# Kernel tuning notes

Hardware: AMD Instinct MI355X
Metric: run time of the kernel (lower is better)

The kernel has to match this reference:

```python
import jax, jax.numpy as jnp
import numpy as np

B, C, Q, E = 32, 1024, 64, 256  # batch, max_context_len, max_question_len, embedding_size
FE = 4 * E                      # final_encoding_size (self_attention=False)


def setup_inputs() -> dict:
    key = jax.random.key(0)
    ks = jax.random.split(key, 7)
    return {
        "context": jax.random.normal(ks[0], (B, C, E), dtype=jnp.float32),
        "question": jax.random.normal(ks[1], (B, Q, E), dtype=jnp.float32),
        "context_mask": jnp.ones((B, C), dtype=jnp.float32),
        "w_question": jax.random.normal(ks[2], (E,), dtype=jnp.float32),
        "w_context": jax.random.normal(ks[3], (E,), dtype=jnp.float32),
        "w_multiple": jax.random.normal(ks[4], (E,), dtype=jnp.float32),
        "final_W": jax.random.normal(ks[5], (FE, FE), dtype=jnp.float32) * (1.0 / np.sqrt(FE)),
        "final_b": jnp.zeros((FE,), dtype=jnp.float32),
    }


def reference(context, question, context_mask, w_question, w_context, w_multiple, final_W, final_b):
    # Trilinear similarity: s[b,c,q] = <w_q, q_q> + <w_c, c_c> + <w_m, c_c * q_q>
    q_weighted = question @ w_question                 # (B, Q)
    ctx_weighted = context @ w_context                 # (B, C)
    # (question.unsqueeze(1) * context.unsqueeze(2)) @ w_multiple, computed
    # without materializing the (B, C, Q, E) intermediate:
    mult = jnp.einsum('bce,bqe->bcq', context * w_multiple, question)  # (B, C, Q)
    similarity = ctx_weighted[:, :, None] + q_weighted[:, None, :] + mult  # (B, C, Q)

    # Context-to-query attention (softmax over question dim)
    c2q_att = jnp.einsum('bcq,bqe->bce', jax.nn.softmax(similarity, axis=2), question)

    # Query-to-context attention (softmax over context dim of row-max scores)
    q2c_weights = jax.nn.softmax(jnp.max(similarity, axis=2), axis=1)   # (B, C)
    q2c_att = jnp.einsum('bc,bce->be', q2c_weights, context)            # (B, E)

    attended = jnp.concatenate(
        [context, c2q_att, context * c2q_att, context * q2c_att[:, None, :]],
        axis=2)                                                          # (B, C, 4E)

    # MaskedLinear: affine map, output rows zeroed where context_mask == 0
    out = (attended @ final_W.T + final_b) * context_mask[:, :, None]    # (B, C, 4E)
    return out
```

## Files before the change

### kernel.cpp

```cpp
#include <hip/hip_runtime.h>

#define BB 32
#define CC 1024
#define QQ 64
#define EE 256
#define FE 1024
#define MM (BB*CC)

typedef __bf16 bf16_t;
typedef bf16_t bf16x8 __attribute__((ext_vector_type(8)));
typedef float f32x4 __attribute__((ext_vector_type(4)));
typedef unsigned short u16x8 __attribute__((ext_vector_type(8)));

__device__ __forceinline__ unsigned short f2bf(float f) {
  unsigned u = __float_as_uint(f);
  u += 0x7fffu + ((u >> 16) & 1u);
  return (unsigned short)(u >> 16);
}
__device__ __forceinline__ float bf2f(unsigned short u) {
  return __uint_as_float(((unsigned)u) << 16);
}

__device__ __forceinline__ void gload_lds16(const void* g, void* l) {
  __builtin_amdgcn_global_load_lds(
      (const __attribute__((address_space(1))) unsigned int*)g,
      (__attribute__((address_space(3))) unsigned int*)l, 16, 0, 0);
}

__global__ void k_prep(const float* __restrict__ question, const float* __restrict__ w_question,
                       float* __restrict__ qw,
                       const float* __restrict__ W, unsigned short* __restrict__ Wb) {
  int bx = blockIdx.x;
  if (bx < 512) {
    int gid = bx * 256 + threadIdx.x;
    int row = gid >> 6;
    int lane = gid & 63;
    const float4 q = *(const float4*)(question + (size_t)row * EE + lane * 4);
    const float4 wq = *(const float4*)(w_question + lane * 4);
    float d = q.x*wq.x + q.y*wq.y + q.z*wq.z + q.w*wq.w;
    d += __shfl_xor(d, 1);  d += __shfl_xor(d, 2);  d += __shfl_xor(d, 4);
    d += __shfl_xor(d, 8);  d += __shfl_xor(d, 16); d += __shfl_xor(d, 32);
    if (lane == 0) qw[row] = d;
  } else {
    int i = ((bx - 512) * 256 + threadIdx.x) * 4;
    float4 v = *(const float4*)(W + i);
    ushort4 o; o.x = f2bf(v.x); o.y = f2bf(v.y); o.z = f2bf(v.z); o.w = f2bf(v.w);
    *(ushort4*)(Wb + i) = o;
  }
}

#define DOT4(acc, A, Bv) acc += A.x*Bv.x + A.y*Bv.y + A.z*Bv.z + A.w*Bv.w

__launch_bounds__(256)
__global__ void k_simpv(const float* __restrict__ ctx, const float* __restrict__ question,
                        const float* __restrict__ qw_g, const float* __restrict__ w_context,
                        const float* __restrict__ w_multiple,
                        float* __restrict__ rowmax, unsigned short* __restrict__ att) {
  __shared__ float qbuf[QQ * 132];
  __shared__ float ck[64][36];
  __shared__ unsigned short Pl[QQ][68];
  __shared__ float cwl[64];
  __shared__ float qwl[QQ];
  const int tid = threadIdx.x;
  const int b = blockIdx.y;
  const int c0 = blockIdx.x * 64;
  const int tx = tid & 15, ty = tid >> 4;

  const float* qb = question + (size_t)b * (QQ * EE);
  if (tid < QQ) qwl[tid] = qw_g[b * QQ + tid];

  const int cr = tid >> 3, er = (tid & 7) * 4;
  const float* crow0 = ctx + ((size_t)(b * CC + c0 + cr)) * EE;
  const float* crow1 = crow0 + 32 * EE;
  unsigned short* arow0 = att + ((size_t)(b * CC + c0 + cr)) * FE;
  unsigned short* arow1 = arow0 + (size_t)32 * FE;
  float s[4][4] = {{0.f}};
  float cp0 = 0.f, cp1 = 0.f;

  for (int h = 0; h < 2; ++h) {
    if (h) __syncthreads();
    for (int idx = tid * 4; idx < QQ * 128; idx += 1024) {
      int row = idx >> 7, col = idx & 127;
      *(float4*)&qbuf[row * 132 + col] = *(const float4*)(qb + (size_t)row * EE + h * 128 + col);
    }
    for (int eo2 = 0; eo2 < 128; eo2 += 32) {
      const int eo = h * 128 + eo2;
      float4 cv0 = *(const float4*)(crow0 + eo + er);
      float4 cv1 = *(const float4*)(crow1 + eo + er);
      float4 wc = *(const float4*)(w_context + eo + er);
      float4 wm = *(const float4*)(w_multiple + eo + er);
      cp0 += cv0.x*wc.x + cv0.y*wc.y + cv0.z*wc.z + cv0.w*wc.w;
      cp1 += cv1.x*wc.x + cv1.y*wc.y + cv1.z*wc.z + cv1.w*wc.w;
      ushort4 u0, u1;
      u0.x = f2bf(cv0.x); u0.y = f2bf(cv0.y); u0.z = f2bf(cv0.z); u0.w = f2bf(cv0.w);
      u1.x = f2bf(cv1.x); u1.y = f2bf(cv1.y); u1.z = f2bf(cv1.z); u1.w = f2bf(cv1.w);
      *(ushort4*)(arow0 + eo + er) = u0;
      *(ushort4*)(arow1 + eo + er) = u1;
      __syncthreads();
      float4 m0, m1;
      m0.x = cv0.x*wm.x; m0.y = cv0.y*wm.y; m0.z = cv0.z*wm.z; m0.w = cv0.w*wm.w;
      m1.x = cv1.x*wm.x; m1.y = cv1.y*wm.y; m1.z = cv1.z*wm.z; m1.w = cv1.w*wm.w;
      *(float4*)&ck[cr][er] = m0;
      *(float4*)&ck[cr + 32][er] = m1;
      __syncthreads();
#pragma unroll
      for (int ee = 0; ee < 32; ee += 4) {
        float4 a0 = *(const float4*)&ck[ty +  0][ee];
        float4 a1 = *(const float4*)&ck[ty + 16][ee];
        float4 a2 = *(const float4*)&ck[ty + 32][ee];
        float4 a3 = *(const float4*)&ck[ty + 48][ee];
        float4 b0 = *(const float4*)&qbuf[(tx +  0) * 132 + eo2 + ee];
        float4 b1 = *(const float4*)&qbuf[(tx + 16) * 132 + eo2 + ee];
        float4 b2 = *(const float4*)&qbuf[(tx + 32) * 132 + eo2 + ee];
        float4 b3 = *(const float4*)&qbuf[(tx + 48) * 132 + eo2 + ee];
        DOT4(s[0][0], a0, b0); DOT4(s[0][1], a0, b1); DOT4(s[0][2], a0, b2); DOT4(s[0][3], a0, b3);
        DOT4(s[1][0], a1, b0); DOT4(s[1][1], a1, b1); DOT4(s[1][2], a1, b2); DOT4(s[1][3], a1, b3);
        DOT4(s[2][0], a2, b0); DOT4(s[2][1], a2, b1); DOT4(s[2][2], a2, b2); DOT4(s[2][3], a2, b3);
        DOT4(s[3][0], a3, b0); DOT4(s[3][1], a3, b1); DOT4(s[3][2], a3, b2); DOT4(s[3][3], a3, b3);
      }
    }
  }
  cp0 += __shfl_xor(cp0, 1); cp0 += __shfl_xor(cp0, 2); cp0 += __shfl_xor(cp0, 4);
  cp1 += __shfl_xor(cp1, 1); cp1 += __shfl_xor(cp1, 2); cp1 += __shfl_xor(cp1, 4);
  if ((tid & 7) == 0) { cwl[cr] = cp0; cwl[cr + 32] = cp1; }
  __syncthreads();

#pragma unroll
  for (int i = 0; i < 4; ++i) {
    int c = ty + 16 * i;
    float cw = cwl[c];
    float f[4], mx = -1e30f;
#pragma unroll
    for (int j = 0; j < 4; ++j) {
      f[j] = s[i][j] + cw + qwl[tx + 16 * j];
      mx = fmaxf(mx, f[j]);
    }
    mx = fmaxf(mx, __shfl_xor(mx, 1));
    mx = fmaxf(mx, __shfl_xor(mx, 2));
    mx = fmaxf(mx, __shfl_xor(mx, 4));
    mx = fmaxf(mx, __shfl_xor(mx, 8));
    float sum = 0.f;
#pragma unroll
    for (int j = 0; j < 4; ++j) { f[j] = expf(f[j] - mx); sum += f[j]; }
    sum += __shfl_xor(sum, 1);
    sum += __shfl_xor(sum, 2);
    sum += __shfl_xor(sum, 4);
    sum += __shfl_xor(sum, 8);
    float inv = 1.f / sum;
    if (tx == 0) rowmax[(size_t)b * CC + c0 + c] = mx;
#pragma unroll
    for (int j = 0; j < 4; ++j) Pl[tx + 16 * j][c] = f2bf(f[j] * inv);
  }
  __syncthreads();

  for (int ep = 0; ep < EE; ep += 64) {
    if (ep) __syncthreads();
    {
      int q = tid >> 2, e16 = (tid & 3) * 16;
      const float* src = qb + (size_t)q * EE + ep + e16;
      *(float4*)&qbuf[q * 68 + e16 +  0] = *(const float4*)(src);
      *(float4*)&qbuf[q * 68 + e16 +  4] = *(const float4*)(src + 4);
      *(float4*)&qbuf[q * 68 + e16 +  8] = *(const float4*)(src + 8);
      *(float4*)&qbuf[q * 68 + e16 + 12] = *(const float4*)(src + 12);
    }
    __syncthreads();
    float s2[4][4] = {{0.f}};
#pragma unroll 8
    for (int q = 0; q < QQ; ++q) {
      float a0 = bf2f(Pl[q][ty +  0]);
      float a1 = bf2f(Pl[q][ty + 16]);
      float a2 = bf2f(Pl[q][ty + 32]);
      float a3 = bf2f(Pl[q][ty + 48]);
      float4 bv = *(const float4*)&qbuf[q * 68 + tx * 4];
      s2[0][0] += a0 * bv.x; s2[0][1] += a0 * bv.y; s2[0][2] += a0 * bv.z; s2[0][3] += a0 * bv.w;
      s2[1][0] += a1 * bv.x; s2[1][1] += a1 * bv.y; s2[1][2] += a1 * bv.z; s2[1][3] += a1 * bv.w;
      s2[2][0] += a2 * bv.x; s2[2][1] += a2 * bv.y; s2[2][2] += a2 * bv.z; s2[2][3] += a2 * bv.w;
      s2[3][0] += a3 * bv.x; s2[3][1] += a3 * bv.y; s2[3][2] += a3 * bv.z; s2[3][3] += a3 * bv.w;
    }
#pragma unroll
    for (int i = 0; i < 4; ++i) {
      int c = ty + 16 * i;
      size_t row = (size_t)(b * CC + c0 + c);
      unsigned short* arow = att + row * (size_t)FE;
      ushort4 cu = *(const ushort4*)(arow + ep + tx * 4);
      float cx = bf2f(cu.x), cy = bf2f(cu.y), cz = bf2f(cu.z), cw = bf2f(cu.w);
      ushort4 o1, o2;
      o1.x = f2bf(s2[i][0]);       o1.y = f2bf(s2[i][1]);       o1.z = f2bf(s2[i][2]);       o1.w = f2bf(s2[i][3]);
      o2.x = f2bf(cx * s2[i][0]);  o2.y = f2bf(cy * s2[i][1]);  o2.z = f2bf(cz * s2[i][2]);  o2.w = f2bf(cw * s2[i][3]);
      *(ushort4*)(arow + 1 * EE + ep + tx * 4) = o1;
      *(ushort4*)(arow + 2 * EE + ep + tx * 4) = o2;
    }
  }
}

__global__ void k_q2c_softmax(const float* __restrict__ rowmax, float* __restrict__ q2cw) {
  int b = blockIdx.x, tid = threadIdx.x;
  __shared__ float rbuf[4], sbuf[4];
  float4 v = *(const float4*)(rowmax + (size_t)b * CC + tid * 4);
  float m = fmaxf(fmaxf(v.x, v.y), fmaxf(v.z, v.w));
  for (int off = 1; off < 64; off <<= 1) m = fmaxf(m, __shfl_xor(m, off));
  int wv = tid >> 6;
  if ((tid & 63) == 0) rbuf[wv] = m;
  __syncthreads();
  m = fmaxf(fmaxf(rbuf[0], rbuf[1]), fmaxf(rbuf[2], rbuf[3]));
  float e0 = expf(v.x - m), e1 = expf(v.y - m), e2 = expf(v.z - m), e3 = expf(v.w - m);
  float sum = e0 + e1 + e2 + e3;
  for (int off = 1; off < 64; off <<= 1) sum += __shfl_xor(sum, off);
  if ((tid & 63) == 0) sbuf[wv] = sum;
  __syncthreads();
  sum = sbuf[0] + sbuf[1] + sbuf[2] + sbuf[3];
  float inv = 1.f / sum;
  float4 o; o.x = e0 * inv; o.y = e1 * inv; o.z = e2 * inv; o.w = e3 * inv;
  *(float4*)(q2cw + (size_t)b * CC + tid * 4) = o;
}

__global__ void k_q2c_part(const unsigned short* __restrict__ att, const float* __restrict__ w,
                           float* __restrict__ part) {
  int b = blockIdx.y, ch = blockIdx.x;
  int e = threadIdx.x;
  const unsigned short* base = att + ((size_t)(b * CC + ch * 128)) * FE + e;
  const float* wp = w + b * CC + ch * 128;
  float acc = 0.f;
#pragma unroll 4
  for (int c = 0; c < 128; ++c) acc += wp[c] * bf2f(base[(size_t)c * FE]);
  part[(b * 8 + ch) * EE + e] = acc;
}

__global__ void k_q2c_sum(const float* __restrict__ part, float* __restrict__ q2catt) {
  int b = blockIdx.x, e = threadIdx.x;
  float a = 0.f;
#pragma unroll
  for (int ch = 0; ch < 8; ++ch) a += part[(b * 8 + ch) * EE + e];
  q2catt[b * EE + e] = a;
}

__global__ void k_att3(const unsigned short* __restrict__ att_ro, const float* __restrict__ q2catt,
                       unsigned short* __restrict__ att_wr) {
  int unit = blockIdx.x * 256 + threadIdx.x;
  int row = unit >> 5;
  int e8 = (unit & 31) * 8;
  int b = row >> 10;
  u16x8 c = *(const u16x8*)(att_ro + (size_t)row * FE + e8);
  float4 g0 = *(const float4*)(q2catt + b * EE + e8);
  float4 g1 = *(const float4*)(q2catt + b * EE + e8 + 4);
  u16x8 o;
  o[0] = f2bf(bf2f(c[0]) * g0.x); o[1] = f2bf(bf2f(c[1]) * g0.y);
  o[2] = f2bf(bf2f(c[2]) * g0.z); o[3] = f2bf(bf2f(c[3]) * g0.w);
  o[4] = f2bf(bf2f(c[4]) * g1.x); o[5] = f2bf(bf2f(c[5]) * g1.y);
  o[6] = f2bf(bf2f(c[6]) * g1.z); o[7] = f2bf(bf2f(c[7]) * g1.w);
  *(u16x8*)(att_wr + (size_t)row * FE + 3 * EE + e8) = o;
}

__launch_bounds__(256, 3)
__global__ void k_gemm(const unsigned short* __restrict__ A, const unsigned short* __restrict__ Bw,
                       const float* __restrict__ bias, const float* __restrict__ mask,
                       float* __restrict__ out) {
  __shared__ bf16_t As[128][32];
  __shared__ bf16_t Bs[128][32];
  const int tid = threadIdx.x;
  const int lane = tid & 63;
  const int wave = tid >> 6;
  const int wr = wave >> 1, wc = wave & 1;

  const int bid = blockIdx.x;
  const int wg = (bid & 7) * 256 + (bid >> 3);
  const int bcol = (wg & 7) * 128;
  const int brow = (wg >> 3) * 128;

  const int r = lane & 15, kg = lane >> 4;
  const int rk = (kg ^ (r & 3)) * 8;

  const int srow = tid >> 2;
  const int sgr = tid & 3;
  const int ssw = (sgr ^ (srow & 3)) * 8;
  const unsigned short* gA0 = A  + (size_t)(brow + srow) * FE + ssw;
  const unsigned short* gA1 = gA0 + (size_t)64 * FE;
  const unsigned short* gB0 = Bw + (size_t)(bcol + srow) * FE + ssw;
  const unsigned short* gB1 = gB0 + (size_t)64 * FE;
  bf16_t* dA0 = &As[srow][sgr * 8];
  bf16_t* dA1 = dA0 + 64 * 32;
  bf16_t* dB0 = &Bs[srow][sgr * 8];
  bf16_t* dB1 = dB0 + 64 * 32;

  f32x4 acc[4][4] = {};

  for (int k0 = 0; k0 < FE; k0 += 32) {
    gload_lds16(gA0 + k0, dA0);
    gload_lds16(gA1 + k0, dA1);
    gload_lds16(gB0 + k0, dB0);
    gload_lds16(gB1 + k0, dB1);
    __syncthreads();
    bf16x8 fa[4], fb[4];
#pragma unroll
    for (int m = 0; m < 4; ++m) fa[m] = *(const bf16x8*)&As[wr * 64 + m * 16 + r][rk];
#pragma unroll
    for (int n = 0; n < 4; ++n) fb[n] = *(const bf16x8*)&Bs[wc * 64 + n * 16 + r][rk];
#pragma unroll
    for (int m = 0; m < 4; ++m)
#pragma unroll
      for (int n = 0; n < 4; ++n)
        acc[m][n] = __builtin_amdgcn_mfma_f32_16x16x32_bf16(fa[m], fb[n], acc[m][n], 0, 0, 0);
    __syncthreads();
  }

#pragma unroll
  for (int m = 0; m < 4; ++m) {
#pragma unroll
    for (int n = 0; n < 4; ++n) {
#pragma unroll
      for (int reg = 0; reg < 4; ++reg) {
        int row = brow + wr * 64 + m * 16 + kg * 4 + reg;
        int col = bcol + wc * 64 + n * 16 + r;
        out[(size_t)row * FE + col] = (acc[m][n][reg] + bias[col]) * mask[row];
      }
    }
  }
}

extern "C" void kernel_launch(void* const* d_in, const int* in_sizes, int n_in,
                              void* d_out, int out_size, void* d_ws, size_t ws_size,
                              hipStream_t stream) {
  const float* ctx  = (const float*)d_in[0];
  const float* ques = (const float*)d_in[1];
  const float* mask = (const float*)d_in[2];
  const float* w_q  = (const float*)d_in[3];
  const float* w_c  = (const float*)d_in[4];
  const float* w_m  = (const float*)d_in[5];
  const float* fW   = (const float*)d_in[6];
  const float* fb   = (const float*)d_in[7];
  float* out = (float*)d_out;

  char* ws = (char*)d_ws;
  float* qw     = (float*)(ws);
  float* rowmax = (float*)(ws + 8192);
  float* q2cw   = (float*)(ws + 139264);
  float* part   = (float*)(ws + 270336);
  float* q2catt = (float*)(ws + 532480);
  unsigned short* attended = (unsigned short*)(ws + 1048576);
  unsigned short* Wb       = (unsigned short*)(ws + 68157440);

  k_prep<<<1536, 256, 0, stream>>>(ques, w_q, qw, fW, Wb);
  k_simpv<<<dim3(16, 32), 256, 0, stream>>>(ctx, ques, qw, w_c, w_m, rowmax, attended);
  k_q2c_softmax<<<32, 256, 0, stream>>>(rowmax, q2cw);
  k_q2c_part<<<dim3(8, 32), 256, 0, stream>>>(attended, q2cw, part);
  k_q2c_sum<<<32, 256, 0, stream>>>(part, q2catt);
  k_att3<<<4096, 256, 0, stream>>>(attended, q2catt, attended);
  k_gemm<<<2048, 256, 0, stream>>>(attended, Wb, fb, mask, out);
}
```

Before: 172.2 us.

## Fuse q2c reduction and context*q2c scaling into GEMM A-tile load

Removes the k_q2c_sum and k_att3 kernels. Each GEMM block now sums the q2c partials for its batch into shared memory. For the last quarter of K it loads the context columns through registers, scales them by the q2c vector, and writes the result to LDS instead of using direct global-to-LDS loads. This saves two launches and one full read/write pass over a quarter of the attended buffer. In exchange, every GEMM block does redundant partial sums, and the register-path loads in the K loop are slower.

```diff
diff --git a/kernel.cpp b/kernel.cpp
--- a/kernel.cpp
+++ b/kernel.cpp
@@ -226,37 +226,13 @@
   part[(b * 8 + ch) * EE + e] = acc;
 }
 
-__global__ void k_q2c_sum(const float* __restrict__ part, float* __restrict__ q2catt) {
-  int b = blockIdx.x, e = threadIdx.x;
-  float a = 0.f;
-#pragma unroll
-  for (int ch = 0; ch < 8; ++ch) a += part[(b * 8 + ch) * EE + e];
-  q2catt[b * EE + e] = a;
-}
-
-__global__ void k_att3(const unsigned short* __restrict__ att_ro, const float* __restrict__ q2catt,
-                       unsigned short* __restrict__ att_wr) {
-  int unit = blockIdx.x * 256 + threadIdx.x;
-  int row = unit >> 5;
-  int e8 = (unit & 31) * 8;
-  int b = row >> 10;
-  u16x8 c = *(const u16x8*)(att_ro + (size_t)row * FE + e8);
-  float4 g0 = *(const float4*)(q2catt + b * EE + e8);
-  float4 g1 = *(const float4*)(q2catt + b * EE + e8 + 4);
-  u16x8 o;
-  o[0] = f2bf(bf2f(c[0]) * g0.x); o[1] = f2bf(bf2f(c[1]) * g0.y);
-  o[2] = f2bf(bf2f(c[2]) * g0.z); o[3] = f2bf(bf2f(c[3]) * g0.w);
-  o[4] = f2bf(bf2f(c[4]) * g1.x); o[5] = f2bf(bf2f(c[5]) * g1.y);
-  o[6] = f2bf(bf2f(c[6]) * g1.z); o[7] = f2bf(bf2f(c[7]) * g1.w);
-  *(u16x8*)(att_wr + (size_t)row * FE + 3 * EE + e8) = o;
-}
-
 __launch_bounds__(256, 3)
 __global__ void k_gemm(const unsigned short* __restrict__ A, const unsigned short* __restrict__ Bw,
-                       const float* __restrict__ bias, const float* __restrict__ mask,
-                       float* __restrict__ out) {
+                       const float* __restrict__ part, const float* __restrict__ bias,
+                       const float* __restrict__ mask, float* __restrict__ out) {
   __shared__ bf16_t As[128][32];
   __shared__ bf16_t Bs[128][32];
+  __shared__ float q2cl[EE];
   const int tid = threadIdx.x;
   const int lane = tid & 63;
   const int wave = tid >> 6;
@@ -266,6 +242,7 @@
   const int wg = (bid & 7) * 256 + (bid >> 3);
   const int bcol = (wg & 7) * 128;
   const int brow = (wg >> 3) * 128;
+  const int bb = brow >> 10;
 
   const int r = lane & 15, kg = lane >> 4;
   const int rk = (kg ^ (r & 3)) * 8;
@@ -282,11 +259,37 @@
   bf16_t* dB0 = &Bs[srow][sgr * 8];
   bf16_t* dB1 = dB0 + 64 * 32;
 
+  {
+    float a = 0.f;
+#pragma unroll
+    for (int ch = 0; ch < 8; ++ch) a += part[(bb * 8 + ch) * EE + tid];
+    q2cl[tid] = a;
+  }
+
   f32x4 acc[4][4] = {};
 
   for (int k0 = 0; k0 < FE; k0 += 32) {
-    gload_lds16(gA0 + k0, dA0);
-    gload_lds16(gA1 + k0, dA1);
+    if (k0 < 768) {
+      gload_lds16(gA0 + k0, dA0);
+      gload_lds16(gA1 + k0, dA1);
+    } else {
+      const int e0 = k0 - 768;
+      u16x8 va = *(const u16x8*)(gA0 + e0);
+      u16x8 vb = *(const u16x8*)(gA1 + e0);
+      float4 g0 = *(const float4*)&q2cl[e0 + ssw];
+      float4 g1 = *(const float4*)&q2cl[e0 + ssw + 4];
+      u16x8 oa, ob;
+      oa[0] = f2bf(bf2f(va[0]) * g0.x); oa[1] = f2bf(bf2f(va[1]) * g0.y);
+      oa[2] = f2bf(bf2f(va[2]) * g0.z); oa[3] = f2bf(bf2f(va[3]) * g0.w);
+      oa[4] = f2bf(bf2f(va[4]) * g1.x); oa[5] = f2bf(bf2f(va[5]) * g1.y);
+      oa[6] = f2bf(bf2f(va[6]) * g1.z); oa[7] = f2bf(bf2f(va[7]) * g1.w);
+      ob[0] = f2bf(bf2f(vb[0]) * g0.x); ob[1] = f2bf(bf2f(vb[1]) * g0.y);
+      ob[2] = f2bf(bf2f(vb[2]) * g0.z); ob[3] = f2bf(bf2f(vb[3]) * g0.w);
+      ob[4] = f2bf(bf2f(vb[4]) * g1.x); ob[5] = f2bf(bf2f(vb[5]) * g1.y);
+      ob[6] = f2bf(bf2f(vb[6]) * g1.z); ob[7] = f2bf(bf2f(vb[7]) * g1.w);
+      *(u16x8*)dA0 = oa;
+      *(u16x8*)dA1 = ob;
+    }
     gload_lds16(gB0 + k0, dB0);
     gload_lds16(gB1 + k0, dB1);
     __syncthreads();
@@ -335,7 +338,6 @@
   float* rowmax = (float*)(ws + 8192);
   float* q2cw   = (float*)(ws + 139264);
   float* part   = (float*)(ws + 270336);
-  float* q2catt = (float*)(ws + 532480);
   unsigned short* attended = (unsigned short*)(ws + 1048576);
   unsigned short* Wb       = (unsigned short*)(ws + 68157440);
 
@@ -343,7 +345,5 @@
   k_simpv<<<dim3(16, 32), 256, 0, stream>>>(ctx, ques, qw, w_c, w_m, rowmax, attended);
   k_q2c_softmax<<<32, 256, 0, stream>>>(rowmax, q2cw);
   k_q2c_part<<<dim3(8, 32), 256, 0, stream>>>(attended, q2cw, part);
-  k_q2c_sum<<<32, 256, 0, stream>>>(part, q2catt);
-  k_att3<<<4096, 256, 0, stream>>>(attended, q2catt, attended);
-  k_gemm<<<2048, 256, 0, stream>>>(attended, Wb, fb, mask, out);
-}
+  k_gemm<<<2048, 256, 0, stream>>>(attended, Wb, part, fb, mask, out);
+}
```

Result: no change. 168.8 us (-1.9%).
